# Kernel tuning notes

Measured on AMD Instinct MI355X. Metric: run time of the kernel, lower is better.

The kernel has to match this reference:

```python
import jax, jax.numpy as jnp
import numpy as np
from jax import lax

V, E, H, L = 32000, 512, 512, 2
B, S, T = 64, 128, 64


def setup_inputs() -> dict:
    key = jax.random.key(0)
    ks = jax.random.split(key, 16)
    sc = 0.05  # weight scale to keep gates/tanh in a sane range
    inp = {
        "tokens": jax.random.randint(ks[0], (T, B), 0, V, dtype=jnp.int32),
        "memory_bank": jax.random.normal(ks[1], (B, S, H), dtype=jnp.float32),
        "lengths": jax.random.randint(ks[2], (B,), 1, S + 1, dtype=jnp.int32),
        "h0": jax.random.normal(ks[3], (L, B, H), dtype=jnp.float32),
        "c0": jax.random.normal(ks[4], (L, B, H), dtype=jnp.float32),
        "embedding": jax.random.normal(ks[5], (V, E), dtype=jnp.float32),
        "w_ih0": jax.random.normal(ks[6], (4 * H, E + H), dtype=jnp.float32) * sc,
        "w_hh0": jax.random.normal(ks[7], (4 * H, H), dtype=jnp.float32) * sc,
        "b_ih0": jax.random.normal(ks[8], (4 * H,), dtype=jnp.float32) * sc,
        "b_hh0": jax.random.normal(ks[9], (4 * H,), dtype=jnp.float32) * sc,
        "w_ih1": jax.random.normal(ks[10], (4 * H, H), dtype=jnp.float32) * sc,
        "w_hh1": jax.random.normal(ks[11], (4 * H, H), dtype=jnp.float32) * sc,
        "b_ih1": jax.random.normal(ks[12], (4 * H,), dtype=jnp.float32) * sc,
        "b_hh1": jax.random.normal(ks[13], (4 * H,), dtype=jnp.float32) * sc,
        "w_in": jax.random.normal(ks[14], (H, H), dtype=jnp.float32) * sc,
        "w_out": jax.random.normal(ks[15], (H, 2 * H), dtype=jnp.float32) * sc,
    }
    return inp


def _lstm_cell(x, h, c, w_ih, w_hh, b_ih, b_hh):
    # PyTorch LSTMCell: gates in (i, f, g, o) order
    g = x @ w_ih.T + b_ih + h @ w_hh.T + b_hh
    i, f, gg, o = jnp.split(g, 4, axis=-1)
    c_new = jax.nn.sigmoid(f) * c + jax.nn.sigmoid(i) * jnp.tanh(gg)
    h_new = jax.nn.sigmoid(o) * jnp.tanh(c_new)
    return h_new, c_new


def reference(tokens, memory_bank, lengths, h0, c0, embedding,
              w_ih0, w_hh0, b_ih0, b_hh0, w_ih1, w_hh1, b_ih1, b_hh1,
              w_in, w_out):
    Bn, Sn, Hn = memory_bank.shape
    mask = jnp.arange(Sn)[None, :] < lengths[:, None]  # [B, S]

    def step(carry, tok):
        h, c, feed = carry  # h, c: [L, B, H]; feed: [B, H]
        emb = jnp.take(embedding, tok, axis=0)           # [B, E]
        x = jnp.concatenate([emb, feed], axis=-1)        # [B, E+H]
        h0n, c0n = _lstm_cell(x, h[0], c[0], w_ih0, w_hh0, b_ih0, b_hh0)
        h1n, c1n = _lstm_cell(h0n, h[1], c[1], w_ih1, w_hh1, b_ih1, b_hh1)
        rnn_out = h1n                                    # [B, H]
        # Luong general attention
        q = rnn_out @ w_in.T                             # [B, H]
        scores = jnp.einsum('bh,bsh->bs', q, memory_bank)
        scores = jnp.where(mask, scores, -jnp.inf)
        p = jax.nn.softmax(scores, axis=-1)              # [B, S]
        ctx = jnp.einsum('bs,bsh->bh', p, memory_bank)   # [B, H]
        attn_h = jnp.tanh(jnp.concatenate([ctx, rnn_out], axis=-1) @ w_out.T)
        new_carry = (jnp.stack([h0n, h1n]), jnp.stack([c0n, c1n]), attn_h)
        return new_carry, (attn_h, p)

    feed0 = jnp.zeros((Bn, Hn), dtype=memory_bank.dtype)
    (h_f, c_f, _), (dec_outs, attns) = lax.scan(step, (h0, c0, feed0), tokens)
    return dec_outs, attns, h_f, c_f
```

## Files before the change

kernel.cpp:

```cpp
#include <hip/hip_runtime.h>
#include <hip/hip_bf16.h>

typedef __bf16 bf16x8 __attribute__((ext_vector_type(8)));
typedef unsigned short u16x8 __attribute__((ext_vector_type(8)));
typedef float f32x4 __attribute__((ext_vector_type(4)));

constexpr int TT = 64;
constexpr int BB = 64;
constexpr int SS = 128;
constexpr int HH = 512;
constexpr int GG = 2048;

constexpr int NW0E = 2048 * 512;
constexpr int NW0R = 2048 * 1024;
constexpr int NW1  = 2048 * 512;
constexpr int NWO  = 512 * 1024;
constexpr int NWI  = 512 * 512;

struct P {
  const int* tok; const float* mbank; const int* len;
  const float* h0_in; const float* c0_in; const float* emb;
  const float* w_ih0; const float* w_hh0; const float* b_ih0; const float* b_hh0;
  const float* w_ih1; const float* w_hh1; const float* b_ih1; const float* b_hh1;
  const float* w_in; const float* w_out;
  float* out_dec; float* out_attn; float* out_hf; float* out_cf;
  unsigned short *W0E, *W0R, *Wih1, *Whh1, *Wout, *WinT;
  float *EGb;
  float *Mw;
  float *b0, *b1, *h0buf, *h1s, *c0s, *c1s, *feed, *part1, *ctx, *scg;
  unsigned int* flag;
};

__device__ __forceinline__ unsigned short f2bf(float f) {
  unsigned int u = __builtin_bit_cast(unsigned int, f);
  return (unsigned short)((u + 0x7fffu + ((u >> 16) & 1u)) >> 16);
}
__device__ __forceinline__ float bf2f(unsigned short h) {
  return __builtin_bit_cast(float, ((unsigned int)h) << 16);
}
__device__ __forceinline__ bf16x8 ldb(const unsigned short* p) {
  return __builtin_bit_cast(bf16x8, *(const u16x8*)p);
}
__device__ __forceinline__ f32x4 mfma_(bf16x8 a, bf16x8 b, f32x4 c) {
  return __builtin_amdgcn_mfma_f32_16x16x32_bf16(a, b, c, 0, 0, 0);
}
__device__ __forceinline__ float sigm(float x) { return 1.f / (1.f + __expf(-x)); }
__device__ __forceinline__ f32x4 zero4() { f32x4 z = {0.f, 0.f, 0.f, 0.f}; return z; }

#define ATL(pp) __hip_atomic_load((pp), __ATOMIC_RELAXED, __HIP_MEMORY_SCOPE_AGENT)
#define ATS(pp, vv) __hip_atomic_store((pp), (vv), __ATOMIC_RELAXED, __HIP_MEMORY_SCOPE_AGENT)
#define ATA(pp, vv) __hip_atomic_fetch_add((pp), (vv), __ATOMIC_RELAXED, __HIP_MEMORY_SCOPE_AGENT)

__device__ __forceinline__ void splitA(const float* s, bf16x8& hi, bf16x8& lo) {
  float4 a0 = *(const float4*)s;
  float4 a1 = *(const float4*)(s + 4);
  float v[8] = {a0.x, a0.y, a0.z, a0.w, a1.x, a1.y, a1.z, a1.w};
  u16x8 h, l;
#pragma unroll
  for (int j = 0; j < 8; ++j) {
    unsigned short hb = f2bf(v[j]);
    h[j] = hb;
    l[j] = f2bf(v[j] - bf2f(hb));
  }
  hi = __builtin_bit_cast(bf16x8, h);
  lo = __builtin_bit_cast(bf16x8, l);
}
__device__ __forceinline__ f32x4 mfma3(bf16x8 ah, bf16x8 al, bf16x8 bh, bf16x8 bl, f32x4 c) {
  c = mfma_(al, bh, c);
  c = mfma_(ah, bl, c);
  c = mfma_(ah, bh, c);
  return c;
}

__global__ void prep_weights(P p) {
  constexpr int TOT = NW0E + NW0R + NW1 + NW1 + NWO + NWI + 2048 + 2048 +
                      32768 * 5 + 8192 + 1024;
  for (int i = blockIdx.x * blockDim.x + threadIdx.x; i < TOT;
       i += gridDim.x * blockDim.x) {
    int j = i;
    float v; unsigned short* dst; int N;
    if (j < NW0E) {
      int n = j >> 9, k = j & 511;
      v = p.w_ih0[n * 1024 + k];
      dst = p.W0E; N = NW0E; goto split;
    }
    j -= NW0E;
    if (j < NW0R) {
      int n = j >> 10, k = j & 1023;
      v = (k < 512) ? p.w_ih0[n * 1024 + 512 + k] : p.w_hh0[n * 512 + (k - 512)];
      dst = p.W0R; N = NW0R; goto split;
    }
    j -= NW0R;
    if (j < NW1) { v = p.w_ih1[j]; dst = p.Wih1; N = NW1; goto split; }
    j -= NW1;
    if (j < NW1) { v = p.w_hh1[j]; dst = p.Whh1; N = NW1; goto split; }
    j -= NW1;
    if (j < NWO) { v = p.w_out[j]; dst = p.Wout; N = NWO; goto split; }
    j -= NWO;
    if (j < NWI) {
      int n = j >> 9, q = j & 511;
      v = p.w_in[q * 512 + n];
      dst = p.WinT; N = NWI; goto split;
    }
    j -= NWI;
    if (j < 2048) { p.b0[j] = p.b_ih0[j] + p.b_hh0[j]; continue; }
    j -= 2048;
    if (j < 2048) { p.b1[j] = p.b_ih1[j] + p.b_hh1[j]; continue; }
    j -= 2048;
    if (j < 32768) { p.h0buf[j] = p.h0_in[j]; continue; }
    j -= 32768;
    if (j < 32768) { p.h1s[j] = p.h0_in[32768 + j]; continue; }
    j -= 32768;
    if (j < 32768) { p.c0s[j] = p.c0_in[j]; continue; }
    j -= 32768;
    if (j < 32768) { p.c1s[j] = p.c0_in[32768 + j]; continue; }
    j -= 32768;
    if (j < 32768) { p.feed[j] = 0.f; continue; }
    j -= 32768;
    if (j < 8192) { p.scg[j] = 0.f; continue; }
    j -= 8192;
    p.flag[j] = 0u;
    continue;
  split:
    {
      unsigned short hb = f2bf(v);
      dst[j] = hb;
      dst[N + j] = f2bf(v - bf2f(hb));
    }
  }
}

__global__ void prep_mw(P p) {
  const int wg = blockIdx.x;
  const int bm = wg & 127, bn = wg >> 7;
  const int tid = threadIdx.x, wave = tid >> 6, lane = tid & 63;
  const int arow = lane & 15, kq = (lane >> 4) * 8;
  const int m0 = bm * 64 + wave * 16;
  const int n0 = bn * 16;
  const float* A = p.mbank + (size_t)(m0 + arow) * HH;
  const unsigned short* Bp = p.WinT + (size_t)(n0 + arow) * HH + kq;
  f32x4 acc = zero4();
  for (int kk = 0; kk < HH; kk += 32) {
    bf16x8 ah, al;
    splitA(A + kk + kq, ah, al);
    acc = mfma3(ah, al, ldb(Bp + kk), ldb(Bp + NWI + kk), acc);
  }
  const int r0 = m0 + (lane >> 4) * 4;
#pragma unroll
  for (int r = 0; r < 4; ++r)
    p.Mw[(size_t)(r0 + r) * HH + n0 + arow] = acc[r];
}

__global__ void prep_eg(P p) {
  const int wg = blockIdx.x;
  const int bn = wg & 127, bm = wg >> 7;
  const int tid = threadIdx.x, wave = tid >> 6, lane = tid & 63;
  const int arow = lane & 15, kq = (lane >> 4) * 8;
  const int m0 = bm * 64 + wave * 16;
  const int n0 = bn * 16;
  const int token = p.tok[m0 + arow];
  const float* A = p.emb + (size_t)token * 512;
  const unsigned short* Bp = p.W0E + (size_t)(n0 + arow) * 512 + kq;
  f32x4 acc = zero4();
  for (int kk = 0; kk < 512; kk += 32) {
    bf16x8 ah, al;
    splitA(A + kk + kq, ah, al);
    acc = mfma3(ah, al, ldb(Bp + kk), ldb(Bp + NW0E + kk), acc);
  }
  const int r0 = m0 + (lane >> 4) * 4;
  const float bb = p.b0[n0 + arow];
#pragma unroll
  for (int r = 0; r < 4; ++r)
    p.EGb[(size_t)(r0 + r) * 2048 + n0 + arow] = acc[r] + bb;
}

__global__ void __launch_bounds__(256) decoder_main(P p) {
  const int wg = blockIdx.x, tid = threadIdx.x;
  const int wave = tid >> 6, lane = tid & 63;
  const int arow = lane & 15;
  const int kq = (lane >> 4) * 8;
  const int g = wg >> 6;
  const int u = wg & 63;
  unsigned nb = 0;

  __shared__ float MwL[32][512];
  __shared__ float Aslab[16][516];
  __shared__ float exch[4][16][16];
  __shared__ float scl[128];
  __shared__ float pl[128];

  const int attb = (g << 4) + (u >> 2);
  const int attq = u & 3;
  for (int idx = tid; idx < 32 * 512; idx += 256) {
    int r = idx >> 9, c = idx & 511;
    MwL[r][c] = p.Mw[(size_t)(attb * 128 + attq * 32 + r) * 512 + c];
  }

  const int w2 = (u < 32) ? u : u - 32;
  const int strip = w2;
  const int gate = wave;
  const int colj = strip * 16 + arow;
  const int rowbase = g * 16 * 512;

  unsigned* slots = p.flag + 128 + g * 128;
  auto gbar = [&]() {
    ++nb;
    asm volatile("s_waitcnt vmcnt(0)" ::: "memory");
    __syncthreads();
    if (tid == 0) ATS(&slots[u], nb);
    for (;;) {
      unsigned v = (tid < 64) ? ATL(&slots[tid]) : nb;
      if (__syncthreads_count((int)(v < nb)) == 0) break;
    }
  };

  auto stageC = [&](const float* base) {
    __syncthreads();
    float4 v[8];
    const float* ap[8];
#pragma unroll
    for (int j = 0; j < 8; ++j) {
      int idx = tid * 4 + j * 1024;
      ap[j] = base + (idx >> 9) * 512 + (idx & 511);
    }
#pragma unroll
    for (int j = 0; j < 8; ++j)
      asm volatile("global_load_dwordx4 %0, %1, off sc1" : "=v"(v[j]) : "v"(ap[j]));
    asm volatile("s_waitcnt vmcnt(0)" ::: "memory");
    __builtin_amdgcn_sched_barrier(0);
#pragma unroll
    for (int j = 0; j < 8; ++j) {
      int idx = tid * 4 + j * 1024;
      *(float4*)&Aslab[idx >> 9][idx & 511] = v[j];
    }
    __syncthreads();
  };
  auto gemm_half = [&](const unsigned short* whi, const unsigned short* wlo,
                       f32x4 acc) {
#pragma unroll 4
    for (int kk = 0; kk < 512; kk += 32) {
      bf16x8 ah, al;
      splitA(&Aslab[arow][kk + kq], ah, al);
      acc = mfma3(ah, al, ldb(whi + kk), ldb(wlo + kk), acc);
    }
    return acc;
  };

  for (int t = 0; t < TT; ++t) {
    const float* h0c = p.h0buf + (t & 1) * (BB * HH);
    float* h0n = p.h0buf + ((t + 1) & 1) * (BB * HH);

    if (u < 32) {
      const size_t wr = (size_t)(gate * 512 + colj) * 1024;
      f32x4 acc = zero4();
      stageC(p.feed + rowbase);
      acc = gemm_half(p.W0R + wr + kq, p.W0R + NW0R + wr + kq, acc);
      stageC(h0c + rowbase);
      acc = gemm_half(p.W0R + wr + 512 + kq, p.W0R + NW0R + wr + 512 + kq, acc);
      const float* eg =
          p.EGb + ((size_t)(t * 64 + g * 16)) * 2048 + gate * 512 + colj;
#pragma unroll
      for (int r = 0; r < 4; ++r) {
        acc[r] += eg[((lane >> 4) * 4 + r) * 2048];
        exch[gate][(lane >> 4) * 4 + r][arow] = acc[r];
      }
      __syncthreads();
      {
        int br = tid >> 4, nc = tid & 15;
        int idx = rowbase + br * 512 + strip * 16 + nc;
        float iv = sigm(exch[0][br][nc]);
        float fv = sigm(exch[1][br][nc]);
        float gv = tanhf(exch[2][br][nc]);
        float ov = sigm(exch[3][br][nc]);
        float cn = fv * p.c0s[idx] + iv * gv;
        p.c0s[idx] = cn;
        float hv = ov * tanhf(cn);
        ATS(&h0n[idx], hv);
        if (t == TT - 1) { p.out_cf[idx] = cn; p.out_hf[idx] = hv; }
      }
    } else {
      const size_t wr = (size_t)(gate * 512 + colj) * 512;
      stageC(p.h1s + rowbase);
      f32x4 acc = gemm_half(p.Whh1 + wr + kq, p.Whh1 + NW1 + wr + kq, zero4());
      const float bb = p.b1[gate * 512 + colj];
#pragma unroll
      for (int r = 0; r < 4; ++r)
        ATS(&p.part1[(g * 16 + (lane >> 4) * 4 + r) * 2048 + gate * 512 + colj],
            acc[r] + bb);
    }
    gbar();

    if (u < 32) {
      const size_t wr = (size_t)(gate * 512 + colj) * 512;
      stageC(h0n + rowbase);
      f32x4 acc = gemm_half(p.Wih1 + wr + kq, p.Wih1 + NW1 + wr + kq, zero4());
#pragma unroll
      for (int r = 0; r < 4; ++r) {
        acc[r] += ATL(&p.part1[(g * 16 + (lane >> 4) * 4 + r) * 2048 +
                               gate * 512 + colj]);
        exch[gate][(lane >> 4) * 4 + r][arow] = acc[r];
      }
      __syncthreads();
      {
        int br = tid >> 4, nc = tid & 15;
        int idx = rowbase + br * 512 + strip * 16 + nc;
        float iv = sigm(exch[0][br][nc]);
        float fv = sigm(exch[1][br][nc]);
        float gv = tanhf(exch[2][br][nc]);
        float ov = sigm(exch[3][br][nc]);
        float cn = fv * p.c1s[idx] + iv * gv;
        p.c1s[idx] = cn;
        float hv = ov * tanhf(cn);
        ATS(&p.h1s[idx], hv);
        if (t == TT - 1) { p.out_cf[BB * HH + idx] = cn; p.out_hf[BB * HH + idx] = hv; }
      }
    } else {
      int base = g * 8192 + (u - 32) * 256 + tid;
      ATS(&p.ctx[base], 0.f);
    }
    gbar();

    {
      float h8[8];
      {
        const float* hp = p.h1s + attb * 512 + lane * 8;
        float4 a, c;
        asm volatile("global_load_dwordx4 %0, %1, off sc1" : "=v"(a) : "v"(hp));
        asm volatile("global_load_dwordx4 %0, %1, off sc1" : "=v"(c) : "v"(hp + 4));
        asm volatile("s_waitcnt vmcnt(0)" ::: "memory");
        __builtin_amdgcn_sched_barrier(0);
        h8[0] = a.x; h8[1] = a.y; h8[2] = a.z; h8[3] = a.w;
        h8[4] = c.x; h8[5] = c.y; h8[6] = c.z; h8[7] = c.w;
      }
#pragma unroll
      for (int i = 0; i < 8; ++i) {
        const int sl = wave * 8 + i;
        const float* mw = &MwL[sl][lane * 8];
        float d = h8[0] * mw[0] + h8[1] * mw[1] + h8[2] * mw[2] + h8[3] * mw[3] +
                  h8[4] * mw[4] + h8[5] * mw[5] + h8[6] * mw[6] + h8[7] * mw[7];
#pragma unroll
        for (int o = 32; o; o >>= 1) d += __shfl_xor(d, o);
        if (lane == 0) ATS(&p.scg[attb * 128 + attq * 32 + sl], d);
      }
      asm volatile("s_waitcnt vmcnt(0)" ::: "memory");
      __syncthreads();
      if (tid == 0) {
        ATA(&p.flag[attb], 1u);
        const unsigned tgt = 4u * (unsigned)(t + 1);
        while (ATL(&p.flag[attb]) < tgt) __builtin_amdgcn_s_sleep(1);
      }
      __syncthreads();
      if (tid < 128) scl[tid] = ATL(&p.scg[attb * 128 + tid]);
      __syncthreads();
      if (wave == 0) {
        const int lenb = p.len[attb];
        float s0 = (lane < lenb) ? scl[lane] : -__builtin_inff();
        float s1 = (lane + 64 < lenb) ? scl[lane + 64] : -__builtin_inff();
        float mx = fmaxf(s0, s1);
#pragma unroll
        for (int o = 32; o; o >>= 1) mx = fmaxf(mx, __shfl_xor(mx, o));
        float e0 = (lane < lenb) ? __expf(s0 - mx) : 0.f;
        float e1 = (lane + 64 < lenb) ? __expf(s1 - mx) : 0.f;
        float sm = e0 + e1;
#pragma unroll
        for (int o = 32; o; o >>= 1) sm += __shfl_xor(sm, o);
        float inv = 1.f / sm;
        pl[lane] = e0 * inv; pl[lane + 64] = e1 * inv;
        if (attq == 0) {
          float* ao = p.out_attn + ((size_t)t * BB + attb) * SS;
          ao[lane] = e0 * inv; ao[lane + 64] = e1 * inv;
        }
      }
      __syncthreads();
      {
        const float* MbB = p.mbank + (size_t)(attb * 128 + attq * 32) * 512;
        const int h2 = tid * 2;
        float2 v[32];
#pragma unroll
        for (int s = 0; s < 32; ++s)
          v[s] = *(const float2*)(MbB + (size_t)s * 512 + h2);
        float ca = 0.f, cb = 0.f;
#pragma unroll
        for (int s = 0; s < 32; ++s) {
          float ps = pl[attq * 32 + s];
          ca += ps * v[s].x;
          cb += ps * v[s].y;
        }
        atomicAdd(&p.ctx[attb * 512 + h2], ca);
        atomicAdd(&p.ctx[attb * 512 + h2 + 1], cb);
      }
    }
    gbar();

    if (u < 8) {
      const int nstrip = u * 4 + wave;
      const int cj = nstrip * 16 + arow;
      const size_t wr = (size_t)cj * 1024;
      f32x4 acc = zero4();
      stageC(p.ctx + rowbase);
      acc = gemm_half(p.Wout + wr + kq, p.Wout + NWO + wr + kq, acc);
      stageC(p.h1s + rowbase);
      acc = gemm_half(p.Wout + wr + 512 + kq, p.Wout + NWO + wr + 512 + kq, acc);
      float* dec = p.out_dec + (size_t)t * BB * HH;
#pragma unroll
      for (int r = 0; r < 4; ++r) {
        int b = g * 16 + (lane >> 4) * 4 + r;
        float v = tanhf(acc[r]);
        dec[b * 512 + cj] = v;
        ATS(&p.feed[b * 512 + cj], v);
      }
    }
    gbar();
  }
}

extern "C" void kernel_launch(void* const* d_in, const int* in_sizes, int n_in,
                              void* d_out, int out_size, void* d_ws, size_t ws_size,
                              hipStream_t stream) {
  P p;
  p.tok   = (const int*)d_in[0];
  p.mbank = (const float*)d_in[1];
  p.len   = (const int*)d_in[2];
  p.h0_in = (const float*)d_in[3];
  p.c0_in = (const float*)d_in[4];
  p.emb   = (const float*)d_in[5];
  p.w_ih0 = (const float*)d_in[6];
  p.w_hh0 = (const float*)d_in[7];
  p.b_ih0 = (const float*)d_in[8];
  p.b_hh0 = (const float*)d_in[9];
  p.w_ih1 = (const float*)d_in[10];
  p.w_hh1 = (const float*)d_in[11];
  p.b_ih1 = (const float*)d_in[12];
  p.b_hh1 = (const float*)d_in[13];
  p.w_in  = (const float*)d_in[14];
  p.w_out = (const float*)d_in[15];

  float* out = (float*)d_out;
  p.out_dec  = out;
  p.out_attn = out + (size_t)TT * BB * HH;
  p.out_hf   = out + (size_t)TT * BB * HH + (size_t)TT * BB * SS;
  p.out_cf   = p.out_hf + 2 * BB * HH;

  char* w = (char*)d_ws;
  auto alloc = [&](size_t n) { char* r = w; w += (n + 255) & ~(size_t)255; return r; };
  p.W0E   = (unsigned short*)alloc((size_t)NW0E * 2 * 2);
  p.W0R   = (unsigned short*)alloc((size_t)NW0R * 2 * 2);
  p.Wih1  = (unsigned short*)alloc((size_t)NW1 * 2 * 2);
  p.Whh1  = (unsigned short*)alloc((size_t)NW1 * 2 * 2);
  p.Wout  = (unsigned short*)alloc((size_t)NWO * 2 * 2);
  p.WinT  = (unsigned short*)alloc((size_t)NWI * 2 * 2);
  p.EGb   = (float*)alloc((size_t)4096 * 2048 * 4);
  p.Mw    = (float*)alloc((size_t)BB * SS * HH * 4);
  p.b0    = (float*)alloc(2048 * 4);
  p.b1    = (float*)alloc(2048 * 4);
  p.h0buf = (float*)alloc((size_t)2 * BB * HH * 4);
  p.h1s   = (float*)alloc((size_t)BB * HH * 4);
  p.c0s   = (float*)alloc((size_t)BB * HH * 4);
  p.c1s   = (float*)alloc((size_t)BB * HH * 4);
  p.feed  = (float*)alloc((size_t)BB * HH * 4);
  p.part1 = (float*)alloc((size_t)BB * GG * 4);
  p.ctx   = (float*)alloc((size_t)BB * HH * 4);
  p.scg   = (float*)alloc((size_t)BB * SS * 4);
  p.flag  = (unsigned int*)alloc(1024 * 4);

  hipLaunchKernelGGL(prep_weights, dim3(4096), dim3(256), 0, stream, p);
  hipLaunchKernelGGL(prep_mw, dim3(4096), dim3(256), 0, stream, p);
  hipLaunchKernelGGL(prep_eg, dim3(8192), dim3(256), 0, stream, p);

  void* args[] = {(void*)&p};
  hipError_t ce = hipLaunchCooperativeKernel((void*)decoder_main, dim3(256),
                                             dim3(256), args, 0, stream);
  if (ce != hipSuccess) {
    (void)hipGetLastError();
    hipLaunchKernelGGL(decoder_main, dim3(256), dim3(256), 0, stream, p);
  }
}
```

Before: 3.854 ms.

## Cache memory-bank slice in LDS as bf16 hi/lo split, Mw rows in registers

Each workgroup keeps its projected-memory (Mw) rows in registers instead of LDS. The freed LDS now holds its 32-row memory_bank slice, stored as a bf16 high/low pair that together approximate fp32. The context accumulation therefore reads the slice from LDS at every decoder step instead of reloading it from global memory. This trades per-step global/L2 traffic for extra VGPR pressure (64 floats per thread) and a little extra ALU to rebuild values from the two bf16 halves, with a small precision loss.

```diff
diff --git a/kernel.cpp b/kernel.cpp
--- a/kernel.cpp
+++ b/kernel.cpp
@@ -183,7 +183,8 @@
   const int u = wg & 63;
   unsigned nb = 0;
 
-  __shared__ float MwL[32][512];
+  __shared__ unsigned short MbHi[32][512];
+  __shared__ unsigned short MbLo[32][512];
   __shared__ float Aslab[16][516];
   __shared__ float exch[4][16][16];
   __shared__ float scl[128];
@@ -191,9 +192,24 @@
 
   const int attb = (g << 4) + (u >> 2);
   const int attq = u & 3;
+
   for (int idx = tid; idx < 32 * 512; idx += 256) {
     int r = idx >> 9, c = idx & 511;
-    MwL[r][c] = p.Mw[(size_t)(attb * 128 + attq * 32 + r) * 512 + c];
+    float v = p.mbank[(size_t)(attb * 128 + attq * 32 + r) * 512 + c];
+    unsigned short hb = f2bf(v);
+    MbHi[r][c] = hb;
+    MbLo[r][c] = f2bf(v - bf2f(hb));
+  }
+  float mwreg[8][8];
+  {
+    const float* mwb = p.Mw + (size_t)(attb * 128 + attq * 32 + wave * 8) * 512 + lane * 8;
+#pragma unroll
+    for (int i = 0; i < 8; ++i) {
+      float4 a = *(const float4*)(mwb + i * 512);
+      float4 b = *(const float4*)(mwb + i * 512 + 4);
+      mwreg[i][0] = a.x; mwreg[i][1] = a.y; mwreg[i][2] = a.z; mwreg[i][3] = a.w;
+      mwreg[i][4] = b.x; mwreg[i][5] = b.y; mwreg[i][6] = b.z; mwreg[i][7] = b.w;
+    }
   }
 
   const int w2 = (u < 32) ? u : u - 32;
@@ -335,9 +351,10 @@
 #pragma unroll
       for (int i = 0; i < 8; ++i) {
         const int sl = wave * 8 + i;
-        const float* mw = &MwL[sl][lane * 8];
-        float d = h8[0] * mw[0] + h8[1] * mw[1] + h8[2] * mw[2] + h8[3] * mw[3] +
-                  h8[4] * mw[4] + h8[5] * mw[5] + h8[6] * mw[6] + h8[7] * mw[7];
+        float d = h8[0] * mwreg[i][0] + h8[1] * mwreg[i][1] +
+                  h8[2] * mwreg[i][2] + h8[3] * mwreg[i][3] +
+                  h8[4] * mwreg[i][4] + h8[5] * mwreg[i][5] +
+                  h8[6] * mwreg[i][6] + h8[7] * mwreg[i][7];
 #pragma unroll
         for (int o = 32; o; o >>= 1) d += __shfl_xor(d, o);
         if (lane == 0) ATS(&p.scg[attb * 128 + attq * 32 + sl], d);
@@ -373,18 +390,17 @@
       }
       __syncthreads();
       {
-        const float* MbB = p.mbank + (size_t)(attb * 128 + attq * 32) * 512;
         const int h2 = tid * 2;
-        float2 v[32];
-#pragma unroll
-        for (int s = 0; s < 32; ++s)
-          v[s] = *(const float2*)(MbB + (size_t)s * 512 + h2);
         float ca = 0.f, cb = 0.f;
-#pragma unroll
+#pragma unroll 4
         for (int s = 0; s < 32; ++s) {
           float ps = pl[attq * 32 + s];
-          ca += ps * v[s].x;
-          cb += ps * v[s].y;
+          unsigned vh = *(const unsigned*)&MbHi[s][h2];
+          unsigned vl = *(const unsigned*)&MbLo[s][h2];
+          ca += ps * (bf2f((unsigned short)(vh & 0xffffu)) +
+                      bf2f((unsigned short)(vl & 0xffffu)));
+          cb += ps * (bf2f((unsigned short)(vh >> 16)) +
+                      bf2f((unsigned short)(vl >> 16)));
         }
         atomicAdd(&p.ctx[attb * 512 + h2], ca);
         atomicAdd(&p.ctx[attb * 512 + h2 + 1], cb);
```

Measured after the change: 3.525 ms. 8.5% less time.
